# Kernel optimization log

Hardware: AMD Instinct MI355X
Metric: run time of the kernel (lower is better)

The kernel has to match this reference:

```python
import jax, jax.numpy as jnp
import numpy as np

B, CIN, COUT, H, W = 2, 256, 256, 96, 96
K, PAD, G = 3, 1, 4           # kernel, padding, deformable_groups
KK = K * K
CG = CIN // G                 # channels per deformable group


def setup_inputs() -> dict:
    key = jax.random.key(0)
    k1, k2, k3, k4 = jax.random.split(key, 4)
    feature = jax.random.normal(k1, (B, CIN, H, W), jnp.float32)
    pred_shape = jax.random.normal(k2, (B, H * W, 4), jnp.float32)
    # init_weights: normal(std=0.01), no biases
    w_offset = jax.random.normal(k3, (G * KK * 2, 4, 1, 1), jnp.float32) * 0.01
    w_deform = jax.random.normal(k4, (COUT, CIN, K, K), jnp.float32) * 0.01
    return {"feature": feature, "pred_shape": pred_shape,
            "w_offset": w_offset, "w_deform": w_deform}


def reference(feature, pred_shape, w_offset, w_deform):
    # pred_shape: (B, H*W, 4) -> (B, 4, H, W); detached in the original
    ps = jnp.transpose(pred_shape, (0, 2, 1)).reshape(B, -1, H, W)
    ps = jax.lax.stop_gradient(ps)
    # 1x1 offset conv: (B, G*2*KK, H, W)
    offset = jnp.einsum('bchw,oc->bohw', ps, w_offset[:, :, 0, 0])
    # mmcv layout per group: [y_k0, x_k0, y_k1, x_k1, ...]
    off = offset.reshape(B, G, KK, 2, H, W)
    off_y, off_x = off[:, :, :, 0], off[:, :, :, 1]   # (B, G, KK, H, W)

    kk = jnp.arange(KK)
    ky = (kk // K).reshape(KK, 1, 1).astype(jnp.float32)
    kx = (kk % K).reshape(KK, 1, 1).astype(jnp.float32)
    yy = jnp.arange(H, dtype=jnp.float32).reshape(1, H, 1)
    xx = jnp.arange(W, dtype=jnp.float32).reshape(1, 1, W)
    # sampling positions (stride=1, dilation=1): (B, G, KK, H, W)
    py = (yy - PAD + ky)[None, None] + off_y
    px = (xx - PAD + kx)[None, None] + off_x

    img = feature.reshape(B, G, CG, H * W)

    def gather(yi, xi):
        # zero outside the image (matches DCN bilinear with zero padding)
        valid = ((yi >= 0) & (yi < H) & (xi >= 0) & (xi < W)).astype(feature.dtype)
        idx = jnp.clip(yi, 0, H - 1) * W + jnp.clip(xi, 0, W - 1)
        v = jnp.take_along_axis(img, idx.reshape(B, G, 1, KK * H * W), axis=3)
        return v.reshape(B, G, CG, KK, H, W) * valid[:, :, None]

    y0 = jnp.floor(py); x0 = jnp.floor(px)
    ly = py - y0; lx = px - x0
    y0i = y0.astype(jnp.int32); x0i = x0.astype(jnp.int32)

    val = ((1 - ly) * (1 - lx))[:, :, None] * gather(y0i, x0i) \
        + ((1 - ly) * lx)[:, :, None] * gather(y0i, x0i + 1) \
        + (ly * (1 - lx))[:, :, None] * gather(y0i + 1, x0i) \
        + (ly * lx)[:, :, None] * gather(y0i + 1, x0i + 1)

    sampled = val.reshape(B, CIN, KK, H, W)
    out = jnp.einsum('bckhw,ock->bohw', sampled, w_deform.reshape(COUT, CIN, KK))
    return jax.nn.relu(out)
```

## Files before the change

kernel.cpp:

```cpp
#include <hip/hip_runtime.h>
#include <hip/hip_bf16.h>
#include <stdint.h>

#define HH   96
#define WW   96
#define HW   9216
#define CIN  256
#define COUT 256
#define NB   2
#define NG   4
#define CG   64
#define KK   9
#define KTOT 2304
#define KB   288
#define TS   8
#define WIN  12
#define SCH  32

typedef __attribute__((ext_vector_type(8))) short short8;
typedef __attribute__((ext_vector_type(4))) float f32x4;
typedef __attribute__((ext_vector_type(4))) uint32_t u32x4;

__device__ __forceinline__ uint32_t pk2bf(float v0, float v1) {
    __hip_bfloat162 h = __float22bfloat162_rn(make_float2(v0, v1));
    uint32_t u;
    __builtin_memcpy(&u, &h, 4);
    return u;
}

__global__ __launch_bounds__(256) void prep_A(const float* __restrict__ wd,
                                              uint16_t* __restrict__ Ablk) {
    int t  = blockIdx.x * 256 + threadIdx.x;
    int kb = t % KB;
    int o  = t / KB;
    int kkA = kb >> 5;
    int c0A = (kb & 31) * 8;
    const float* src = wd + (size_t)o * KTOT + c0A * KK + kkA;
    float a[8];
#pragma unroll
    for (int e = 0; e < 8; ++e) a[e] = src[e * KK];
    uint16_t* dst = Ablk + ((size_t)kb * 256 + o) * 8;
    u32x4 v;
    v.x = pk2bf(a[0], a[1]);
    v.y = pk2bf(a[2], a[3]);
    v.z = pk2bf(a[4], a[5]);
    v.w = pk2bf(a[6], a[7]);
    *(u32x4*)dst = v;
}

__global__ __launch_bounds__(256) void sampler(const float* __restrict__ feature,
                                               const float* __restrict__ pred,
                                               const float* __restrict__ woff,
                                               uint16_t* __restrict__ S) {
    __shared__ float ft[SCH * WIN * WIN];

    int tid = threadIdx.x;
    int cb = blockIdx.y, b = blockIdx.z;
    int ch0 = cb * SCH;
    int g = ch0 >> 6;
    int ty = blockIdx.x / (WW / TS), tx = blockIdx.x % (WW / TS);
    int r0 = ty * TS, c0 = tx * TS;
    int rlo = min(max(r0 - 2, 0), HH - WIN);
    int clo = min(max(c0 - 2, 0), WW - WIN);

    const float* fg = feature + ((size_t)(b * CIN + ch0)) * HW;
    for (int e = tid; e < SCH * WIN * WIN; e += 256) {
        int ch = e / (WIN * WIN);
        int re = e - ch * (WIN * WIN);
        int rr = re / WIN, cc = re - rr * WIN;
        ft[e] = fg[(size_t)ch * HW + (rlo + rr) * WW + clo + cc];
    }
    __syncthreads();

    int lane = tid & 63, wv = tid >> 6;
    int lr = lane >> 3, lc = lane & 7;
    int hy = r0 + lr, hx = c0 + lc;
    int p = hy * WW + hx;
    float4 ps4 = *(const float4*)(pred + ((size_t)b * HW + p) * 4);

    const float* ftw = ft + (wv * 8) * (WIN * WIN);
    const float* fgw = fg + (size_t)(wv * 8) * HW;
    int kb_base = cb * 4 + wv;

#pragma unroll
    for (int kk = 0; kk < KK; ++kk) {
        const float* wy = woff + (g * KK + kk) * 8;
        float offy = ps4.x * wy[0] + ps4.y * wy[1] + ps4.z * wy[2] + ps4.w * wy[3];
        float offx = ps4.x * wy[4] + ps4.y * wy[5] + ps4.z * wy[6] + ps4.w * wy[7];
        float py = (float)(hy - 1 + kk / 3) + offy;
        float px = (float)(hx - 1 + kk % 3) + offx;
        float fy = floorf(py), fx = floorf(px);
        int y0 = (int)fy, x0 = (int)fx;
        float ly = py - fy, lx = px - fx;
        int r = min(max(y0, 0), HH - 2);
        int q = min(max(x0, 0), WW - 2);
        float wyA = (y0 == r) ? (1.f - ly) : ((y0 == -1) ? ly : 0.f);
        float wyB = (y0 == r) ? ly : ((y0 == HH - 1) ? (1.f - ly) : 0.f);
        float wxA = (x0 == q) ? (1.f - lx) : ((x0 == -1) ? lx : 0.f);
        float wxB = (x0 == q) ? lx : ((x0 == WW - 1) ? (1.f - lx) : 0.f);
        float c00 = wyA * wxA, c01 = wyA * wxB;
        float c10 = wyB * wxA, c11 = wyB * wxB;

        bool fast = (r >= rlo) & (r <= rlo + WIN - 2) &
                    (q >= clo) & (q <= clo + WIN - 2);

        uint16_t* Sp = S + (((size_t)b * KB + (kk * 32 + kb_base)) * HW + p) * 8;
        uint32_t pk[4];

        if (fast) {
            int base = (r - rlo) * WIN + (q - clo);
#pragma unroll
            for (int ep = 0; ep < 4; ++ep) {
                const float* f0 = ftw + (2 * ep) * (WIN * WIN) + base;
                const float* f1 = f0 + (WIN * WIN);
                float v0 = c00 * f0[0] + c01 * f0[1] + c10 * f0[WIN] + c11 * f0[WIN + 1];
                float v1 = c00 * f1[0] + c01 * f1[1] + c10 * f1[WIN] + c11 * f1[WIN + 1];
                pk[ep] = pk2bf(v0, v1);
            }
        } else {
            size_t gb = (size_t)r * WW + q;
#pragma unroll
            for (int ep = 0; ep < 4; ++ep) {
                const float* f0 = fgw + (size_t)(2 * ep) * HW + gb;
                const float* f1 = f0 + HW;
                float v0 = c00 * f0[0] + c01 * f0[1] + c10 * f0[WW] + c11 * f0[WW + 1];
                float v1 = c00 * f1[0] + c01 * f1[1] + c10 * f1[WW] + c11 * f1[WW + 1];
                pk[ep] = pk2bf(v0, v1);
            }
        }
        u32x4 vv = {pk[0], pk[1], pk[2], pk[3]};
        *(u32x4*)(Sp) = vv;
    }
}

__global__ __launch_bounds__(256, 3) void gemm_kernel(const uint16_t* __restrict__ S,
                                                      const uint16_t* __restrict__ Ablk,
                                                      float* __restrict__ out) {
    __shared__ uint16_t sB[2][8 * 64 * 8];

    int tid = threadIdx.x;
    int lane = tid & 63, wv = tid >> 6;
    int wr = wv >> 1, wc = wv & 1;
    int col0 = blockIdx.x * 64;
    int o0   = blockIdx.y * 128;
    int b    = blockIdx.z;

    const uint16_t* Bg = S + (size_t)b * KB * HW * 8;

    f32x4 acc[4][2];
#pragma unroll
    for (int m = 0; m < 4; ++m)
#pragma unroll
        for (int n = 0; n < 2; ++n) acc[m][n] = (f32x4){0.f, 0.f, 0.f, 0.f};

    int kc = lane >> 4, il = lane & 15;
    const int NT = KTOT / 64;

    const uint16_t* Arow = Ablk + ((size_t)(o0 + wr * 64 + il)) * 8;

    auto LOADA = [&](int t, short8 (&af)[2][4]) {
#pragma unroll
        for (int h = 0; h < 2; ++h)
#pragma unroll
            for (int m = 0; m < 4; ++m)
                af[h][m] = *(const short8*)(Arow + ((size_t)(t * 8 + h * 4 + kc) * 256 + m * 16) * 8);
    };

    auto STAGEB = [&](int t, int buf) {
#pragma unroll
        for (int j = 0; j < 2; ++j) {
            int kb = t * 8 + wv * 2 + j;
            int lc_ = wv * 2 + j;
            __builtin_amdgcn_global_load_lds(
                (const __attribute__((address_space(1))) uint32_t*)
                    (Bg + ((size_t)kb * HW + col0 + lane) * 8),
                (__attribute__((address_space(3))) uint32_t*)
                    (&sB[buf][(lc_ * 64 + lane) * 8]),
                16, 0, 0);
        }
    };

    short8 afA[2][4], afB[2][4];

    LOADA(0, afA);
    STAGEB(0, 0);
    STAGEB(1, 1);

    auto ITER = [&](int t, short8 (&use)[2][4], short8 (&next)[2][4], int buf) {
        if (t < NT - 1) {
            asm volatile("s_waitcnt vmcnt(2)\n\ts_barrier" ::: "memory");
        } else {
            asm volatile("s_waitcnt vmcnt(0)\n\ts_barrier" ::: "memory");
        }
        __builtin_amdgcn_sched_barrier(0);

        if (t + 1 < NT) LOADA(t + 1, next);

        short8 bf[2][2];
#pragma unroll
        for (int h = 0; h < 2; ++h)
#pragma unroll
            for (int n = 0; n < 2; ++n)
                bf[h][n] = *(const short8*)(&sB[buf][((h * 4 + kc) * 64 + wc * 32 + n * 16 + il) * 8]);

#pragma unroll
        for (int h = 0; h < 2; ++h)
#pragma unroll
            for (int m = 0; m < 4; ++m)
#pragma unroll
                for (int n = 0; n < 2; ++n)
                    acc[m][n] = __builtin_amdgcn_mfma_f32_16x16x32_bf16(use[h][m], bf[h][n], acc[m][n], 0, 0, 0);

        asm volatile("s_waitcnt lgkmcnt(0)\n\ts_barrier" ::: "memory");
        __builtin_amdgcn_sched_barrier(0);
        if (t + 2 < NT) STAGEB(t + 2, buf);
    };

    for (int tt = 0; tt < NT; tt += 2) {
        ITER(tt,     afA, afB, 0);
        ITER(tt + 1, afB, afA, 1);
    }

    int r4 = (lane >> 4) * 4;
    size_t obase = ((size_t)b * COUT + o0 + wr * 64) * HW + col0 + wc * 32;
#pragma unroll
    for (int m = 0; m < 4; ++m)
#pragma unroll
        for (int n = 0; n < 2; ++n)
#pragma unroll
            for (int r = 0; r < 4; ++r) {
                float v = acc[m][n][r];
                v = v > 0.f ? v : 0.f;
                out[obase + (size_t)(m * 16 + r4 + r) * HW + n * 16 + il] = v;
            }
}

extern "C" void kernel_launch(void* const* d_in, const int* in_sizes, int n_in,
                              void* d_out, int out_size, void* d_ws, size_t ws_size,
                              hipStream_t stream) {
    (void)in_sizes; (void)n_in; (void)out_size; (void)ws_size;
    const float* feature = (const float*)d_in[0];
    const float* pred    = (const float*)d_in[1];
    const float* woff    = (const float*)d_in[2];
    const float* wdef    = (const float*)d_in[3];
    float* out = (float*)d_out;

    const size_t S_BYTES = (size_t)NB * KB * HW * 8 * 2;
    uint16_t* S    = (uint16_t*)d_ws;
    uint16_t* Ablk = (uint16_t*)((char*)d_ws + S_BYTES);

    hipLaunchKernelGGL(prep_A, dim3(288), dim3(256), 0, stream, wdef, Ablk);
    hipLaunchKernelGGL(sampler, dim3((HH / TS) * (WW / TS), CIN / SCH, NB), dim3(256), 0, stream,
                       feature, pred, woff, S);
    hipLaunchKernelGGL(gemm_kernel, dim3(HW / 64, COUT / 128, NB), dim3(256), 0, stream,
                       S, Ablk, out);
}
```

Before: 86.92 us.

## Rewrite GEMM as single-wave blocks loading straight to registers with XCD-aware tile mapping

The GEMM kernel moves from 256-thread blocks that stage B through LDS with barriers to 64-thread single-wave blocks. Each wave computes a 64x64 output tile with both A and B fragments loaded directly from global memory into registers, double-buffered with no LDS or barriers. Block IDs are remapped so the four output-channel tiles sharing a column strip land on the same XCD, which improves L2 reuse of B. The tradeoffs are more redundant global loads per tile, since there is no sharing across waves, and higher register pressure from 16 accumulators plus two register buffers.

```diff
diff --git a/kernel.cpp b/kernel.cpp
--- a/kernel.cpp
+++ b/kernel.cpp
@@ -133,100 +133,77 @@
     }
 }
 
-__global__ __launch_bounds__(256, 3) void gemm_kernel(const uint16_t* __restrict__ S,
-                                                      const uint16_t* __restrict__ Ablk,
-                                                      float* __restrict__ out) {
-    __shared__ uint16_t sB[2][8 * 64 * 8];
-
-    int tid = threadIdx.x;
-    int lane = tid & 63, wv = tid >> 6;
-    int wr = wv >> 1, wc = wv & 1;
-    int col0 = blockIdx.x * 64;
-    int o0   = blockIdx.y * 128;
-    int b    = blockIdx.z;
-
-    const uint16_t* Bg = S + (size_t)b * KB * HW * 8;
-
-    f32x4 acc[4][2];
+__global__ __launch_bounds__(64, 2) void gemm_kernel(const uint16_t* __restrict__ S,
+                                                     const uint16_t* __restrict__ Ablk,
+                                                     float* __restrict__ out) {
+    int lane = threadIdx.x;
+    int bid = blockIdx.x;
+    int xcd = bid & 7;
+    int j   = bid >> 3;
+    int my  = j & 3;
+    int pairid = xcd * 36 + (j >> 2);
+    int b  = pairid / 144;
+    int py = pairid % 144;
+    int o0 = my * 64, col0 = py * 64;
+    int kc = lane >> 4, il = lane & 15;
+
+    const uint16_t* Ap = Ablk + ((size_t)kc * 256 + o0 + il) * 8;
+    const uint16_t* Bp = S + (size_t)b * KB * HW * 8 + ((size_t)kc * HW + col0 + il) * 8;
+    const size_t Astep = (size_t)4 * 256 * 8;
+    const size_t Bstep = (size_t)4 * HW * 8;
+
+    f32x4 acc[4][4];
 #pragma unroll
     for (int m = 0; m < 4; ++m)
 #pragma unroll
-        for (int n = 0; n < 2; ++n) acc[m][n] = (f32x4){0.f, 0.f, 0.f, 0.f};
-
-    int kc = lane >> 4, il = lane & 15;
-    const int NT = KTOT / 64;
-
-    const uint16_t* Arow = Ablk + ((size_t)(o0 + wr * 64 + il)) * 8;
-
-    auto LOADA = [&](int t, short8 (&af)[2][4]) {
-#pragma unroll
-        for (int h = 0; h < 2; ++h)
-#pragma unroll
-            for (int m = 0; m < 4; ++m)
-                af[h][m] = *(const short8*)(Arow + ((size_t)(t * 8 + h * 4 + kc) * 256 + m * 16) * 8);
-    };
-
-    auto STAGEB = [&](int t, int buf) {
-#pragma unroll
-        for (int j = 0; j < 2; ++j) {
-            int kb = t * 8 + wv * 2 + j;
-            int lc_ = wv * 2 + j;
-            __builtin_amdgcn_global_load_lds(
-                (const __attribute__((address_space(1))) uint32_t*)
-                    (Bg + ((size_t)kb * HW + col0 + lane) * 8),
-                (__attribute__((address_space(3))) uint32_t*)
-                    (&sB[buf][(lc_ * 64 + lane) * 8]),
-                16, 0, 0);
-        }
-    };
-
-    short8 afA[2][4], afB[2][4];
-
-    LOADA(0, afA);
-    STAGEB(0, 0);
-    STAGEB(1, 1);
-
-    auto ITER = [&](int t, short8 (&use)[2][4], short8 (&next)[2][4], int buf) {
-        if (t < NT - 1) {
-            asm volatile("s_waitcnt vmcnt(2)\n\ts_barrier" ::: "memory");
-        } else {
-            asm volatile("s_waitcnt vmcnt(0)\n\ts_barrier" ::: "memory");
-        }
-        __builtin_amdgcn_sched_barrier(0);
-
-        if (t + 1 < NT) LOADA(t + 1, next);
-
-        short8 bf[2][2];
-#pragma unroll
-        for (int h = 0; h < 2; ++h)
-#pragma unroll
-            for (int n = 0; n < 2; ++n)
-                bf[h][n] = *(const short8*)(&sB[buf][((h * 4 + kc) * 64 + wc * 32 + n * 16 + il) * 8]);
-
-#pragma unroll
-        for (int h = 0; h < 2; ++h)
-#pragma unroll
-            for (int m = 0; m < 4; ++m)
-#pragma unroll
-                for (int n = 0; n < 2; ++n)
-                    acc[m][n] = __builtin_amdgcn_mfma_f32_16x16x32_bf16(use[h][m], bf[h][n], acc[m][n], 0, 0, 0);
-
-        asm volatile("s_waitcnt lgkmcnt(0)\n\ts_barrier" ::: "memory");
-        __builtin_amdgcn_sched_barrier(0);
-        if (t + 2 < NT) STAGEB(t + 2, buf);
-    };
+        for (int n = 0; n < 4; ++n) acc[m][n] = (f32x4){0.f, 0.f, 0.f, 0.f};
+
+    const int NT = KTOT / 32;
+
+    short8 a0[4], b0[4], a1[4], b1[4];
+
+#define LOADT(t, areg, breg)                                                   \
+    {                                                                          \
+        const uint16_t* ap = Ap + (size_t)(t) * Astep;                         \
+        const uint16_t* bp = Bp + (size_t)(t) * Bstep;                         \
+        areg[0] = *(const short8*)(ap + 0 * 16 * 8);                           \
+        areg[1] = *(const short8*)(ap + 1 * 16 * 8);                           \
+        areg[2] = *(const short8*)(ap + 2 * 16 * 8);                           \
+        areg[3] = *(const short8*)(ap + 3 * 16 * 8);                           \
+        breg[0] = *(const short8*)(bp + 0 * 16 * 8);                           \
+        breg[1] = *(const short8*)(bp + 1 * 16 * 8);                           \
+        breg[2] = *(const short8*)(bp + 2 * 16 * 8);                           \
+        breg[3] = *(const short8*)(bp + 3 * 16 * 8);                           \
+    }
+
+#define MFMAT(areg, breg)                                                      \
+    {                                                                          \
+        _Pragma("unroll")                                                      \
+        for (int m = 0; m < 4; ++m)                                            \
+            _Pragma("unroll")                                                  \
+            for (int n = 0; n < 4; ++n)                                        \
+                acc[m][n] = __builtin_amdgcn_mfma_f32_16x16x32_bf16(           \
+                    areg[m], breg[n], acc[m][n], 0, 0, 0);                     \
+    }
+
+    LOADT(0, a0, b0);
+    LOADT(1, a1, b1);
 
     for (int tt = 0; tt < NT; tt += 2) {
-        ITER(tt,     afA, afB, 0);
-        ITER(tt + 1, afB, afA, 1);
-    }
-
-    int r4 = (lane >> 4) * 4;
-    size_t obase = ((size_t)b * COUT + o0 + wr * 64) * HW + col0 + wc * 32;
+        MFMAT(a0, b0);
+        if (tt + 2 < NT) LOADT(tt + 2, a0, b0);
+        MFMAT(a1, b1);
+        if (tt + 3 < NT) LOADT(tt + 3, a1, b1);
+    }
+#undef LOADT
+#undef MFMAT
+
+    int r4 = kc * 4;
+    size_t obase = ((size_t)b * COUT + o0) * HW + col0;
 #pragma unroll
     for (int m = 0; m < 4; ++m)
 #pragma unroll
-        for (int n = 0; n < 2; ++n)
+        for (int n = 0; n < 4; ++n)
 #pragma unroll
             for (int r = 0; r < 4; ++r) {
                 float v = acc[m][n][r];
@@ -252,6 +229,6 @@
     hipLaunchKernelGGL(prep_A, dim3(288), dim3(256), 0, stream, wdef, Ablk);
     hipLaunchKernelGGL(sampler, dim3((HH / TS) * (WW / TS), CIN / SCH, NB), dim3(256), 0, stream,
                        feature, pred, woff, S);
-    hipLaunchKernelGGL(gemm_kernel, dim3(HW / 64, COUT / 128, NB), dim3(256), 0, stream,
+    hipLaunchKernelGGL(gemm_kernel, dim3(8 * (HW / 64) * NB / 8 * 4), dim3(64), 0, stream,
                        S, Ablk, out);
 }
```

Measured after the change: 77.12 us. -11.3%, faster.
